# Optimization experiments

Measured on AMD Instinct MI355X. Metric: run time of the kernel, lower is better.

## Reference

```python
import jax, jax.numpy as jnp
import numpy as np

B, T, D = 2, 2048, 1024
D_LABEL = D // 2
N_LABELS = 50


def setup_inputs() -> dict:
    key = jax.random.key(0)
    ks = jax.random.split(key, 10)
    dep = jax.random.normal(ks[0], (B, T, D), dtype=jnp.float32)
    head = jax.random.normal(ks[1], (B, T + 1, D), dtype=jnp.float32)
    head_indices = jax.random.randint(ks[2], (B, T), 0, T + 1)
    mask = jnp.ones((B, T), dtype=bool)
    # learned params
    lim_p = 1.0 / np.sqrt(D)
    dep_W = jax.random.uniform(ks[3], (D_LABEL, D), minval=-lim_p, maxval=lim_p, dtype=jnp.float32)
    dep_b = jax.random.uniform(ks[4], (D_LABEL,), minval=-lim_p, maxval=lim_p, dtype=jnp.float32)
    head_W = jax.random.uniform(ks[5], (D_LABEL, D), minval=-lim_p, maxval=lim_p, dtype=jnp.float32)
    head_b = jax.random.uniform(ks[6], (D_LABEL,), minval=-lim_p, maxval=lim_p, dtype=jnp.float32)
    # xavier_uniform over last two dims of W
    lim_w = np.sqrt(6.0 / (D_LABEL + D_LABEL))
    W = jax.random.uniform(ks[7], (N_LABELS, D_LABEL, D_LABEL), minval=-lim_w, maxval=lim_w, dtype=jnp.float32)
    bias = jnp.zeros((N_LABELS,), dtype=jnp.float32)
    return {"dep": dep, "head": head, "head_indices": head_indices, "mask": mask,
            "dep_W": dep_W, "dep_b": dep_b, "head_W": head_W, "head_b": head_b,
            "W": W, "bias": bias}


def reference(dep, head, head_indices, mask, dep_W, dep_b, head_W, head_b, W, bias):
    # project to label space [B,T,d_label] / [B,T+1,d_label]
    dep_label = jnp.einsum('btd,ed->bte', dep, dep_W) + dep_b
    head_label = jnp.einsum('btd,ed->bte', head, head_W) + head_b
    # gather predicted head rep per token: [B,T,d_label]
    selected = jnp.take_along_axis(head_label, head_indices[..., None], axis=1)
    # biaffine scoring: dep^T W_n head for each label n -> [B,T,n_labels]
    logits = jnp.einsum('btd,nde,bte->btn', dep_label, W, selected)
    return logits + bias[None, None, :]
```

## Files before the change

### kernel.cpp

```cpp
#include <hip/hip_runtime.h>
#include <hip/hip_bf16.h>
#include <cstdint>

typedef __bf16 bf16;
typedef bf16 bf16x8 __attribute__((ext_vector_type(8)));
typedef float f32x4 __attribute__((ext_vector_type(4)));

#define NTOK 4096
#define DLBL 512
#define NLAB 50

__device__ inline bf16x8 cvt8(float4 a, float4 b) {
  bf16x8 r;
  r[0] = (bf16)a.x; r[1] = (bf16)a.y; r[2] = (bf16)a.z; r[3] = (bf16)a.w;
  r[4] = (bf16)b.x; r[5] = (bf16)b.y; r[6] = (bf16)b.z; r[7] = (bf16)b.w;
  return r;
}

__device__ __forceinline__ void gl16(const bf16* g, void* l) {
  __builtin_amdgcn_global_load_lds(
      (const __attribute__((address_space(1))) void*)g,
      (__attribute__((address_space(3))) void*)l, 16, 0, 0);
}

__global__ __launch_bounds__(256) void convW_k(const float* __restrict__ W,
                                               bf16* __restrict__ Wb) {
  int i = blockIdx.x * 256 + threadIdx.x;
  const float4* s = (const float4*)W + (size_t)i * 2;
  float4 a = s[0], b = s[1];
  *(bf16x8*)(Wb + (size_t)i * 8) = cvt8(a, b);
}

__global__ __launch_bounds__(256) void projA_k(const float* __restrict__ Wp,
                                               const float* __restrict__ X,
                                               const float* __restrict__ bv,
                                               bf16* __restrict__ outT) {
  __shared__ char lds[15360];
  char* ldsA = lds;
  char* ldsB = lds + 10240;
  const int tid = threadIdx.x, l = tid & 63, w = tid >> 6;
  const int tokbase = blockIdx.y * 64;
  const int ebase   = blockIdx.x * 128;
  const int wr = w & 1, wc = w >> 1;
  f32x4 acc[4][2] = {};
  const int arow = tid >> 1, ahalf = tid & 1;
  const int brow = tid >> 2, bgr = tid & 3;
  const float* aS = Wp + (size_t)(ebase + arow) * 1024 + ahalf * 16;
  const float* bS = X  + (size_t)(tokbase + brow) * 1024 + bgr * 8;
  const int lo = (l & 15) * 80 + (l >> 4) * 16;
  for (int kb = 0; kb < 1024; kb += 32) {
    float4 a0 = *(const float4*)(aS + kb);
    float4 a1 = *(const float4*)(aS + kb + 4);
    float4 a2 = *(const float4*)(aS + kb + 8);
    float4 a3 = *(const float4*)(aS + kb + 12);
    float4 b0 = *(const float4*)(bS + kb);
    float4 b1 = *(const float4*)(bS + kb + 4);
    *(bf16x8*)(ldsA + arow * 80 + ahalf * 32)      = cvt8(a0, a1);
    *(bf16x8*)(ldsA + arow * 80 + ahalf * 32 + 16) = cvt8(a2, a3);
    *(bf16x8*)(ldsB + brow * 80 + bgr * 16)        = cvt8(b0, b1);
    __syncthreads();
    bf16x8 aF[4], bF[2];
#pragma unroll
    for (int i = 0; i < 4; ++i) aF[i] = *(bf16x8*)(ldsA + (wr * 64 + i * 16) * 80 + lo);
#pragma unroll
    for (int j = 0; j < 2; ++j) bF[j] = *(bf16x8*)(ldsB + (wc * 32 + j * 16) * 80 + lo);
#pragma unroll
    for (int i = 0; i < 4; ++i)
#pragma unroll
      for (int j = 0; j < 2; ++j)
        acc[i][j] = __builtin_amdgcn_mfma_f32_16x16x32_bf16(aF[i], bF[j], acc[i][j], 0, 0, 0);
    __syncthreads();
  }
#pragma unroll
  for (int i = 0; i < 4; ++i)
#pragma unroll
    for (int j = 0; j < 2; ++j)
#pragma unroll
      for (int r = 0; r < 4; ++r) {
        int eg = ebase + wr * 64 + i * 16 + (l >> 4) * 4 + r;
        int tg = tokbase + wc * 32 + j * 16 + (l & 15);
        outT[(size_t)eg * NTOK + tg] = (bf16)(acc[i][j][r] + bv[eg]);
      }
}

__global__ __launch_bounds__(256) void projB_k(const float* __restrict__ head,
                                               const int* __restrict__ hidx,
                                               const float* __restrict__ Wp,
                                               const float* __restrict__ bv,
                                               bf16* __restrict__ selO) {
  __shared__ char lds[15360];
  char* ldsA = lds;
  char* ldsB = lds + 10240;
  const int tid = threadIdx.x, l = tid & 63, w = tid >> 6;
  const int tokbase = blockIdx.y * 128;
  const int ebase   = blockIdx.x * 64;
  const int wr = w & 1, wc = w >> 1;
  f32x4 acc[4][2] = {};
  const int arow = tid >> 1, ahalf = tid & 1;
  const int brow = tid >> 2, bgr = tid & 3;
  const int flat = tokbase + arow;
  const int bb = flat >> 11;
  const int hv = hidx[flat];
  const float* aS = head + ((size_t)bb * 2049 + hv) * 1024 + ahalf * 16;
  const float* bS = Wp + (size_t)(ebase + brow) * 1024 + bgr * 8;
  const int lo = (l & 15) * 80 + (l >> 4) * 16;
  for (int kb = 0; kb < 1024; kb += 32) {
    float4 a0 = *(const float4*)(aS + kb);
    float4 a1 = *(const float4*)(aS + kb + 4);
    float4 a2 = *(const float4*)(aS + kb + 8);
    float4 a3 = *(const float4*)(aS + kb + 12);
    float4 b0 = *(const float4*)(bS + kb);
    float4 b1 = *(const float4*)(bS + kb + 4);
    *(bf16x8*)(ldsA + arow * 80 + ahalf * 32)      = cvt8(a0, a1);
    *(bf16x8*)(ldsA + arow * 80 + ahalf * 32 + 16) = cvt8(a2, a3);
    *(bf16x8*)(ldsB + brow * 80 + bgr * 16)        = cvt8(b0, b1);
    __syncthreads();
    bf16x8 aF[4], bF[2];
#pragma unroll
    for (int i = 0; i < 4; ++i) aF[i] = *(bf16x8*)(ldsA + (wr * 64 + i * 16) * 80 + lo);
#pragma unroll
    for (int j = 0; j < 2; ++j) bF[j] = *(bf16x8*)(ldsB + (wc * 32 + j * 16) * 80 + lo);
#pragma unroll
    for (int i = 0; i < 4; ++i)
#pragma unroll
      for (int j = 0; j < 2; ++j)
        acc[i][j] = __builtin_amdgcn_mfma_f32_16x16x32_bf16(aF[i], bF[j], acc[i][j], 0, 0, 0);
    __syncthreads();
  }
#pragma unroll
  for (int i = 0; i < 4; ++i)
#pragma unroll
    for (int j = 0; j < 2; ++j)
#pragma unroll
      for (int r = 0; r < 4; ++r) {
        int tg = tokbase + wr * 64 + i * 16 + (l >> 4) * 4 + r;
        int eg = ebase + wc * 32 + j * 16 + (l & 15);
        selO[(size_t)tg * DLBL + eg] = (bf16)(acc[i][j][r] + bv[eg]);
      }
}

__global__ __launch_bounds__(512, 4) void biaff_k(const bf16* __restrict__ Wb,
                                                  const bf16* __restrict__ sel,
                                                  const bf16* __restrict__ depT,
                                                  float* __restrict__ parts) {
  __shared__ char lds[73728];
  const int tid = threadIdx.x, l = tid & 63, w = tid >> 6;

  const int lin = blockIdx.x;
  const int xcd = lin & 7, idx = lin >> 3;
  const int sub = idx % 25;
  const int bx  = idx / 25;
  const int combo = xcd * 25 + sub;
  const int n  = combo % 50;
  const int dz = combo / 50;
  const int tokbase = bx * 256;
  const int dbase   = dz * 128;

  const int wd = w >> 2, wt = w & 3;
  f32x4 acc[4][4] = {};

  const int srow = l >> 2;
  const int schunk = ((l & 3) ^ ((l >> 3) & 3)) * 8;
  const bf16* aG = Wb  + ((size_t)(n * DLBL + dbase + w * 16 + srow)) * DLBL + schunk;
  const bf16* bG = sel + ((size_t)(tokbase + w * 32 + srow)) * DLBL + schunk;
  const int aOff = w * 1024;
  const int bOff = 8192 + w * 2048;

  const int lq = l & 15, lh = l >> 4;
  const int ro = lh ^ ((lq >> 1) & 3);
  const char* rdA = lds + (wd * 64 + lq) * 64 + ro * 16;
  const char* rdB = lds + 8192 + (wt * 64 + lq) * 64 + ro * 16;

#define STG(T) do { \
    const bf16* a_ = aG + (T) * 32; \
    const bf16* b_ = bG + (T) * 32; \
    char* la_ = lds + ((T) % 3) * 24576 + aOff; \
    char* lb_ = lds + ((T) % 3) * 24576 + bOff; \
    gl16(a_, la_); \
    gl16(b_, lb_); \
    gl16(b_ + 16 * DLBL, lb_ + 1024); \
  } while (0)
#define WAITV(N) asm volatile("s_waitcnt vmcnt(" #N ")" ::: "memory")
#define PHASE(T, DOSTG, DOWV3, DOWV0, DOBAR) do { \
    const char* cA = rdA + ((T) % 3) * 24576; \
    const char* cB = rdB + ((T) % 3) * 24576; \
    bf16x8 aF[4], bF[4]; \
    aF[0] = *(const bf16x8*)(cA + 0 * 1024); \
    aF[1] = *(const bf16x8*)(cA + 1 * 1024); \
    aF[2] = *(const bf16x8*)(cA + 2 * 1024); \
    aF[3] = *(const bf16x8*)(cA + 3 * 1024); \
    bF[0] = *(const bf16x8*)(cB + 0 * 1024); \
    bF[1] = *(const bf16x8*)(cB + 1 * 1024); \
    bF[2] = *(const bf16x8*)(cB + 2 * 1024); \
    bF[3] = *(const bf16x8*)(cB + 3 * 1024); \
    if (DOSTG) STG((T) + 2); \
    __builtin_amdgcn_s_setprio(1); \
    _Pragma("unroll") \
    for (int i = 0; i < 4; ++i) \
      _Pragma("unroll") \
      for (int j = 0; j < 4; ++j) \
        acc[i][j] = __builtin_amdgcn_mfma_f32_16x16x32_bf16(aF[i], bF[j], acc[i][j], 0, 0, 0); \
    __builtin_amdgcn_s_setprio(0); \
    if (DOWV3) WAITV(3); \
    if (DOWV0) WAITV(0); \
    if (DOBAR) __builtin_amdgcn_s_barrier(); \
  } while (0)

  STG(0); STG(1);
  WAITV(3);
  __builtin_amdgcn_s_barrier();

  PHASE(0, 1, 1, 0, 1);  PHASE(1, 1, 1, 0, 1);  PHASE(2, 1, 1, 0, 1);
  PHASE(3, 1, 1, 0, 1);  PHASE(4, 1, 1, 0, 1);  PHASE(5, 1, 1, 0, 1);
  PHASE(6, 1, 1, 0, 1);  PHASE(7, 1, 1, 0, 1);  PHASE(8, 1, 1, 0, 1);
  PHASE(9, 1, 1, 0, 1);  PHASE(10, 1, 1, 0, 1); PHASE(11, 1, 1, 0, 1);
  PHASE(12, 1, 1, 0, 1); PHASE(13, 1, 1, 0, 1);
  PHASE(14, 0, 0, 1, 1);
  PHASE(15, 0, 0, 0, 0);

#undef PHASE
#undef WAITV
#undef STG

  float p[4] = {0.f, 0.f, 0.f, 0.f};
#pragma unroll
  for (int j = 0; j < 4; ++j) {
    const int tg = tokbase + wt * 64 + j * 16 + lq;
#pragma unroll
    for (int i = 0; i < 4; ++i)
#pragma unroll
      for (int r = 0; r < 4; ++r) {
        int dg = dbase + wd * 64 + i * 16 + lh * 4 + r;
        p[j] += acc[i][j][r] * (float)depT[(size_t)dg * NTOK + tg];
      }
  }
#pragma unroll
  for (int j = 0; j < 4; ++j) {
    p[j] += __shfl_xor(p[j], 16);
    p[j] += __shfl_xor(p[j], 32);
  }
  if (l < 16) {
#pragma unroll
    for (int j = 0; j < 4; ++j) {
      int tg = tokbase + wt * 64 + j * 16 + l;
      parts[(size_t)(dz * 2 + wd) * 204800 + (size_t)tg * NLAB + n] = p[j];
    }
  }
}

__global__ __launch_bounds__(256) void fin_k(const float* __restrict__ parts,
                                             const float* __restrict__ bias,
                                             float* __restrict__ out) {
  int i = blockIdx.x * 256 + threadIdx.x;
  float v = 0.f;
#pragma unroll
  for (int q = 0; q < 8; ++q) v += parts[(size_t)q * 204800 + i];
  out[i] = v + bias[i % NLAB];
}

extern "C" void kernel_launch(void* const* d_in, const int* in_sizes, int n_in,
                              void* d_out, int out_size, void* d_ws, size_t ws_size,
                              hipStream_t stream) {
  const float* dep    = (const float*)d_in[0];
  const float* head   = (const float*)d_in[1];
  const int*   hidx   = (const int*)d_in[2];
  const float* dep_W  = (const float*)d_in[4];
  const float* dep_b  = (const float*)d_in[5];
  const float* head_W = (const float*)d_in[6];
  const float* head_b = (const float*)d_in[7];
  const float* W      = (const float*)d_in[8];
  const float* bias   = (const float*)d_in[9];
  float* out = (float*)d_out;

  char* ws = (char*)d_ws;
  bf16*  Wb    = (bf16*)(ws);
  bf16*  depT  = (bf16*)(ws + 26214400);
  bf16*  selB  = (bf16*)(ws + 30408704);
  float* parts = (float*)(ws + 34603008);
  if (ws_size < (size_t)41156608) return;

  hipLaunchKernelGGL(convW_k, dim3(6400), dim3(256), 0, stream, W, Wb);
  hipLaunchKernelGGL(projA_k, dim3(4, 64), dim3(256), 0, stream, dep_W, dep, dep_b, depT);
  hipLaunchKernelGGL(projB_k, dim3(8, 32), dim3(256), 0, stream, head, hidx, head_W, head_b, selB);
  hipLaunchKernelGGL(biaff_k, dim3(3200), dim3(512), 0, stream, Wb, selB, depT, parts);
  hipLaunchKernelGGL(fin_k, dim3(800), dim3(256), 0, stream, parts, bias, out);
}
```

Measured before the change: 194.2 us.

## Merge prep kernels into one launch and double per-wave tile in biaffine kernel

The W conversion and the two projection kernels become one prep kernel that dispatches on block index, removing two launches and letting the three independent jobs overlap. The biaffine kernel drops from 8 to 4 waves per block, and each wave now computes a 64x128 tile (4x8 MFMA accumulators) instead of 64x64. Each wave issues twice as many global-to-LDS loads per stage, with the wait counts adjusted to match. This raises register pressure and lowers the wave count per block in exchange for more fragment reuse and fewer LDS reads per MFMA.

```diff
diff --git a/kernel.cpp b/kernel.cpp
--- a/kernel.cpp
+++ b/kernel.cpp
@@ -23,24 +23,15 @@
       (__attribute__((address_space(3))) void*)l, 16, 0, 0);
 }
 
-__global__ __launch_bounds__(256) void convW_k(const float* __restrict__ W,
-                                               bf16* __restrict__ Wb) {
-  int i = blockIdx.x * 256 + threadIdx.x;
-  const float4* s = (const float4*)W + (size_t)i * 2;
-  float4 a = s[0], b = s[1];
-  *(bf16x8*)(Wb + (size_t)i * 8) = cvt8(a, b);
-}
-
-__global__ __launch_bounds__(256) void projA_k(const float* __restrict__ Wp,
-                                               const float* __restrict__ X,
-                                               const float* __restrict__ bv,
-                                               bf16* __restrict__ outT) {
-  __shared__ char lds[15360];
+__device__ void projA_body(int bidx, const float* __restrict__ Wp,
+                           const float* __restrict__ X,
+                           const float* __restrict__ bv,
+                           bf16* __restrict__ outT, char* lds) {
   char* ldsA = lds;
   char* ldsB = lds + 10240;
   const int tid = threadIdx.x, l = tid & 63, w = tid >> 6;
-  const int tokbase = blockIdx.y * 64;
-  const int ebase   = blockIdx.x * 128;
+  const int tokbase = (bidx >> 2) * 64;
+  const int ebase   = (bidx & 3) * 128;
   const int wr = w & 1, wc = w >> 1;
   f32x4 acc[4][2] = {};
   const int arow = tid >> 1, ahalf = tid & 1;
@@ -83,17 +74,16 @@
       }
 }
 
-__global__ __launch_bounds__(256) void projB_k(const float* __restrict__ head,
-                                               const int* __restrict__ hidx,
-                                               const float* __restrict__ Wp,
-                                               const float* __restrict__ bv,
-                                               bf16* __restrict__ selO) {
-  __shared__ char lds[15360];
+__device__ void projB_body(int bidx, const float* __restrict__ head,
+                           const int* __restrict__ hidx,
+                           const float* __restrict__ Wp,
+                           const float* __restrict__ bv,
+                           bf16* __restrict__ selO, char* lds) {
   char* ldsA = lds;
   char* ldsB = lds + 10240;
   const int tid = threadIdx.x, l = tid & 63, w = tid >> 6;
-  const int tokbase = blockIdx.y * 128;
-  const int ebase   = blockIdx.x * 64;
+  const int tokbase = (bidx >> 3) * 128;
+  const int ebase   = (bidx & 7) * 64;
   const int wr = w & 1, wc = w >> 1;
   f32x4 acc[4][2] = {};
   const int arow = tid >> 1, ahalf = tid & 1;
@@ -139,7 +129,32 @@
       }
 }
 
-__global__ __launch_bounds__(512, 4) void biaff_k(const bf16* __restrict__ Wb,
+__global__ __launch_bounds__(256) void prep_k(const float* __restrict__ W,
+                                              bf16* __restrict__ Wb,
+                                              const float* __restrict__ dep_W,
+                                              const float* __restrict__ dep,
+                                              const float* __restrict__ dep_b,
+                                              bf16* __restrict__ depT,
+                                              const float* __restrict__ head,
+                                              const int* __restrict__ hidx,
+                                              const float* __restrict__ head_W,
+                                              const float* __restrict__ head_b,
+                                              bf16* __restrict__ selB) {
+  __shared__ char lds[15360];
+  const int b = blockIdx.x;
+  if (b < 256) {
+    projA_body(b, dep_W, dep, dep_b, depT, lds);
+  } else if (b < 512) {
+    projB_body(b - 256, head, hidx, head_W, head_b, selB, lds);
+  } else {
+    int i = (b - 512) * 256 + threadIdx.x;
+    const float4* s = (const float4*)W + (size_t)i * 2;
+    float4 a = s[0], c = s[1];
+    *(bf16x8*)(Wb + (size_t)i * 8) = cvt8(a, c);
+  }
+}
+
+__global__ __launch_bounds__(256, 2) void biaff_k(const bf16* __restrict__ Wb,
                                                   const bf16* __restrict__ sel,
                                                   const bf16* __restrict__ depT,
                                                   float* __restrict__ parts) {
@@ -156,58 +171,54 @@
   const int tokbase = bx * 256;
   const int dbase   = dz * 128;
 
-  const int wd = w >> 2, wt = w & 3;
-  f32x4 acc[4][4] = {};
+  const int wd = w >> 1, wt = w & 1;
+  f32x4 acc[4][8] = {};
 
   const int srow = l >> 2;
   const int schunk = ((l & 3) ^ ((l >> 3) & 3)) * 8;
-  const bf16* aG = Wb  + ((size_t)(n * DLBL + dbase + w * 16 + srow)) * DLBL + schunk;
-  const bf16* bG = sel + ((size_t)(tokbase + w * 32 + srow)) * DLBL + schunk;
-  const int aOff = w * 1024;
-  const int bOff = 8192 + w * 2048;
+  const bf16* aG = Wb  + ((size_t)(n * DLBL + dbase + w * 32 + srow)) * DLBL + schunk;
+  const bf16* bG = sel + ((size_t)(tokbase + w * 64 + srow)) * DLBL + schunk;
+  const int aOff = w * 2048;
+  const int bOff = 8192 + w * 4096;
 
   const int lq = l & 15, lh = l >> 4;
   const int ro = lh ^ ((lq >> 1) & 3);
   const char* rdA = lds + (wd * 64 + lq) * 64 + ro * 16;
-  const char* rdB = lds + 8192 + (wt * 64 + lq) * 64 + ro * 16;
+  const char* rdB = lds + 8192 + (wt * 128 + lq) * 64 + ro * 16;
 
 #define STG(T) do { \
     const bf16* a_ = aG + (T) * 32; \
     const bf16* b_ = bG + (T) * 32; \
     char* la_ = lds + ((T) % 3) * 24576 + aOff; \
     char* lb_ = lds + ((T) % 3) * 24576 + bOff; \
-    gl16(a_, la_); \
-    gl16(b_, lb_); \
-    gl16(b_ + 16 * DLBL, lb_ + 1024); \
+    gl16(a_, la_);            gl16(a_ + 16 * DLBL, la_ + 1024); \
+    gl16(b_, lb_);            gl16(b_ + 16 * DLBL, lb_ + 1024); \
+    gl16(b_ + 32 * DLBL, lb_ + 2048); gl16(b_ + 48 * DLBL, lb_ + 3072); \
   } while (0)
 #define WAITV(N) asm volatile("s_waitcnt vmcnt(" #N ")" ::: "memory")
-#define PHASE(T, DOSTG, DOWV3, DOWV0, DOBAR) do { \
+#define PHASE(T, DOSTG, DOWV6, DOWV0, DOBAR) do { \
     const char* cA = rdA + ((T) % 3) * 24576; \
     const char* cB = rdB + ((T) % 3) * 24576; \
-    bf16x8 aF[4], bF[4]; \
-    aF[0] = *(const bf16x8*)(cA + 0 * 1024); \
-    aF[1] = *(const bf16x8*)(cA + 1 * 1024); \
-    aF[2] = *(const bf16x8*)(cA + 2 * 1024); \
-    aF[3] = *(const bf16x8*)(cA + 3 * 1024); \
-    bF[0] = *(const bf16x8*)(cB + 0 * 1024); \
-    bF[1] = *(const bf16x8*)(cB + 1 * 1024); \
-    bF[2] = *(const bf16x8*)(cB + 2 * 1024); \
-    bF[3] = *(const bf16x8*)(cB + 3 * 1024); \
+    bf16x8 aF[4], bF[8]; \
+    _Pragma("unroll") \
+    for (int i = 0; i < 4; ++i) aF[i] = *(const bf16x8*)(cA + i * 1024); \
+    _Pragma("unroll") \
+    for (int j = 0; j < 8; ++j) bF[j] = *(const bf16x8*)(cB + j * 1024); \
     if (DOSTG) STG((T) + 2); \
     __builtin_amdgcn_s_setprio(1); \
     _Pragma("unroll") \
     for (int i = 0; i < 4; ++i) \
       _Pragma("unroll") \
-      for (int j = 0; j < 4; ++j) \
+      for (int j = 0; j < 8; ++j) \
         acc[i][j] = __builtin_amdgcn_mfma_f32_16x16x32_bf16(aF[i], bF[j], acc[i][j], 0, 0, 0); \
     __builtin_amdgcn_s_setprio(0); \
-    if (DOWV3) WAITV(3); \
+    if (DOWV6) WAITV(6); \
     if (DOWV0) WAITV(0); \
     if (DOBAR) __builtin_amdgcn_s_barrier(); \
   } while (0)
 
   STG(0); STG(1);
-  WAITV(3);
+  WAITV(6);
   __builtin_amdgcn_s_barrier();
 
   PHASE(0, 1, 1, 0, 1);  PHASE(1, 1, 1, 0, 1);  PHASE(2, 1, 1, 0, 1);
@@ -222,10 +233,10 @@
 #undef WAITV
 #undef STG
 
-  float p[4] = {0.f, 0.f, 0.f, 0.f};
-#pragma unroll
-  for (int j = 0; j < 4; ++j) {
-    const int tg = tokbase + wt * 64 + j * 16 + lq;
+  float p[8] = {0.f, 0.f, 0.f, 0.f, 0.f, 0.f, 0.f, 0.f};
+#pragma unroll
+  for (int j = 0; j < 8; ++j) {
+    const int tg = tokbase + wt * 128 + j * 16 + lq;
 #pragma unroll
     for (int i = 0; i < 4; ++i)
 #pragma unroll
@@ -235,14 +246,14 @@
       }
   }
 #pragma unroll
-  for (int j = 0; j < 4; ++j) {
+  for (int j = 0; j < 8; ++j) {
     p[j] += __shfl_xor(p[j], 16);
     p[j] += __shfl_xor(p[j], 32);
   }
   if (l < 16) {
 #pragma unroll
-    for (int j = 0; j < 4; ++j) {
-      int tg = tokbase + wt * 64 + j * 16 + l;
+    for (int j = 0; j < 8; ++j) {
+      int tg = tokbase + wt * 128 + j * 16 + l;
       parts[(size_t)(dz * 2 + wd) * 204800 + (size_t)tg * NLAB + n] = p[j];
     }
   }
@@ -279,9 +290,8 @@
   float* parts = (float*)(ws + 34603008);
   if (ws_size < (size_t)41156608) return;
 
-  hipLaunchKernelGGL(convW_k, dim3(6400), dim3(256), 0, stream, W, Wb);
-  hipLaunchKernelGGL(projA_k, dim3(4, 64), dim3(256), 0, stream, dep_W, dep, dep_b, depT);
-  hipLaunchKernelGGL(projB_k, dim3(8, 32), dim3(256), 0, stream, head, hidx, head_W, head_b, selB);
-  hipLaunchKernelGGL(biaff_k, dim3(3200), dim3(512), 0, stream, Wb, selB, depT, parts);
+  hipLaunchKernelGGL(prep_k, dim3(6912), dim3(256), 0, stream,
+                     W, Wb, dep_W, dep, dep_b, depT, head, hidx, head_W, head_b, selB);
+  hipLaunchKernelGGL(biaff_k, dim3(3200), dim3(256), 0, stream, Wb, selB, depT, parts);
   hipLaunchKernelGGL(fin_k, dim3(800), dim3(256), 0, stream, parts, bias, out);
 }
```

Result: faster. 163.3 us (-15.9%).
